# Kernel optimization log

Measured on AMD Instinct MI355X. Metric: run time of the kernel, lower is better.

## Reference

```python
import jax, jax.numpy as jnp
import numpy as np

N = 100000   # nodes
E = 600000   # edges
D_IN, D_H, D_OUT = 128, 128, 128


def glorot(key, shape):
    lim = float(np.sqrt(6.0 / (shape[0] + shape[1])))
    return jax.random.uniform(key, shape, jnp.float32, -lim, lim)


def setup_inputs() -> dict:
    key = jax.random.key(0)
    k1, k2, k3, k4 = jax.random.split(key, 4)
    x = jax.random.normal(k1, (N, D_IN), jnp.float32)
    edge_index = jax.random.randint(k2, (2, E), 0, N, jnp.int64)
    W1 = glorot(k3, (D_IN, D_H))
    b1 = jnp.zeros((D_H,), jnp.float32)
    W2 = glorot(k4, (D_H, D_OUT))
    b2 = jnp.zeros((D_OUT,), jnp.float32)
    return {"x": x, "W1": W1, "b1": b1, "W2": W2, "b2": b2, "edge_index": edge_index}


def gcn_conv(x, W, b, src, dst, n):
    # GCNConv: D^{-1/2}(A+I)D^{-1/2} X W + b  (self loops already in src/dst)
    h = x @ W                                   # [N, d_out]
    ones = jnp.ones(src.shape[0], h.dtype)
    deg = jax.ops.segment_sum(ones, dst, num_segments=n)      # in-degree incl self loop
    dinv = jnp.where(deg > 0, jax.lax.rsqrt(deg), 0.0)        # deg^{-1/2}
    norm = dinv[src] * dinv[dst]                              # [E+N]
    msgs = h[src] * norm[:, None]                             # gather + scale
    out = jax.ops.segment_sum(msgs, dst, num_segments=n)      # scatter-add to targets
    return out + b


def reference(x, W1, b1, W2, b2, edge_index):
    loop = jnp.arange(N, dtype=edge_index.dtype)
    src = jnp.concatenate([edge_index[0], loop])
    dst = jnp.concatenate([edge_index[1], loop])
    h = gcn_conv(x, W1, b1, src, dst, N)
    h = jax.nn.relu(h)  # dropout is a no-op in eval mode
    return gcn_conv(h, W2, b2, src, dst, N)
```

## Files before the change

kernel.cpp:

```cpp
#include <hip/hip_runtime.h>

#define NFEAT 128

typedef __attribute__((ext_vector_type(8))) short bf16x8;
typedef __attribute__((ext_vector_type(4))) float f32x4;

__device__ inline ushort f2b(float v) {
  unsigned u = __builtin_bit_cast(unsigned, v);
  return (ushort)((u + 0x7FFFu + ((u >> 16) & 1u)) >> 16);
}

__device__ inline void agg_accum(const ushort* __restrict__ h,
                                 const int2* __restrict__ csr2, int e, int end, int c,
                                 float& a0, float& a1, float& a2, float& a3) {
  for (; e < end; e += 4) {
    int4 q0 = *(const int4*)(csr2 + e);
    int4 q1 = *(const int4*)(csr2 + e + 2);
    uint2 h0 = *(const uint2*)(h + (size_t)q0.x * NFEAT + c);
    uint2 h1 = *(const uint2*)(h + (size_t)q0.z * NFEAT + c);
    uint2 h2 = *(const uint2*)(h + (size_t)q1.x * NFEAT + c);
    uint2 h3 = *(const uint2*)(h + (size_t)q1.z * NFEAT + c);
    float w0 = __int_as_float(q0.y), w1 = __int_as_float(q0.w);
    float w2 = __int_as_float(q1.y), w3 = __int_as_float(q1.w);
    a0 = fmaf(w0, __uint_as_float(h0.x << 16), a0);
    a1 = fmaf(w0, __uint_as_float(h0.x & 0xffff0000u), a1);
    a2 = fmaf(w0, __uint_as_float(h0.y << 16), a2);
    a3 = fmaf(w0, __uint_as_float(h0.y & 0xffff0000u), a3);
    a0 = fmaf(w1, __uint_as_float(h1.x << 16), a0);
    a1 = fmaf(w1, __uint_as_float(h1.x & 0xffff0000u), a1);
    a2 = fmaf(w1, __uint_as_float(h1.y << 16), a2);
    a3 = fmaf(w1, __uint_as_float(h1.y & 0xffff0000u), a3);
    a0 = fmaf(w2, __uint_as_float(h2.x << 16), a0);
    a1 = fmaf(w2, __uint_as_float(h2.x & 0xffff0000u), a1);
    a2 = fmaf(w2, __uint_as_float(h2.y << 16), a2);
    a3 = fmaf(w2, __uint_as_float(h2.y & 0xffff0000u), a3);
    a0 = fmaf(w3, __uint_as_float(h3.x << 16), a0);
    a1 = fmaf(w3, __uint_as_float(h3.x & 0xffff0000u), a1);
    a2 = fmaf(w3, __uint_as_float(h3.y << 16), a2);
    a3 = fmaf(w3, __uint_as_float(h3.y & 0xffff0000u), a3);
  }
}

__global__ __launch_bounds__(256) void k_cast_w(const float* __restrict__ W1,
                                                const float* __restrict__ W2,
                                                ushort* __restrict__ WT1,
                                                ushort* __restrict__ WT2) {
  int b = blockIdx.x;
  const float* W = (b < 64) ? W1 : W2;
  ushort* WT = (b < 64) ? WT1 : WT2;
  int idx = (b & 63) * 256 + threadIdx.x;
  int k = idx >> 7, nn = idx & 127;
  WT[nn * 128 + k] = f2b(W[idx]);
}


__global__ __launch_bounds__(256) void k_par1(const float* __restrict__ x,
                                              const ushort* __restrict__ WT1,
                                              ushort* __restrict__ h1, int n,
                                              const int* __restrict__ dst,
                                              int* __restrict__ cnt, int E,
                                              int gemmBlocks) {
  if ((int)blockIdx.x >= gemmBlocks) {
    int bid = blockIdx.x - gemmBlocks;
    int range = bid & 7, chunk = bid >> 3;
    int lo = (int)(((long long)range * n) >> 3);
    int hi = (int)(((long long)(range + 1) * n) >> 3);
    int i = chunk * 1024 + threadIdx.x * 4;
    if (i + 3 < E) {
      int4 d4 = *(const int4*)(dst + i);
      if ((unsigned)(d4.x - lo) < (unsigned)(hi - lo)) atomicAdd(&cnt[d4.x], 1);
      if ((unsigned)(d4.y - lo) < (unsigned)(hi - lo)) atomicAdd(&cnt[d4.y], 1);
      if ((unsigned)(d4.z - lo) < (unsigned)(hi - lo)) atomicAdd(&cnt[d4.z], 1);
      if ((unsigned)(d4.w - lo) < (unsigned)(hi - lo)) atomicAdd(&cnt[d4.w], 1);
    } else {
      for (int j = 0; j < 4; j++) {
        if (i + j < E) {
          int d = dst[i + j];
          if ((unsigned)(d - lo) < (unsigned)(hi - lo)) atomicAdd(&cnt[d], 1);
        }
      }
    }
    return;
  }
  __shared__ ushort sW[128][136];
  int tid = threadIdx.x;
  {
    int r = tid >> 1, hh = tid & 1;
    const uint4* srcp = (const uint4*)(WT1 + r * 128 + hh * 64);
    uint4* dstp = (uint4*)(&sW[r][hh * 64]);
#pragma unroll
    for (int j = 0; j < 8; j++) dstp[j] = srcp[j];
  }
  __syncthreads();

  int wave = tid >> 6;
  int lane = tid & 63;
  int l16 = lane & 15;
  int quad = lane >> 4;
  int rowBase = blockIdx.x * 128 + wave * 32;

  bf16x8 afrag[2][4];
#pragma unroll
  for (int rt = 0; rt < 2; rt++) {
    int row = rowBase + rt * 16 + l16;
    row = min(row, n - 1);
    const float* Ap = x + (size_t)row * NFEAT + quad * 8;
#pragma unroll
    for (int ks = 0; ks < 4; ks++) {
      float4 f0 = *(const float4*)(Ap + ks * 32);
      float4 f1 = *(const float4*)(Ap + ks * 32 + 4);
      ushort t[8] = {f2b(f0.x), f2b(f0.y), f2b(f0.z), f2b(f0.w),
                     f2b(f1.x), f2b(f1.y), f2b(f1.z), f2b(f1.w)};
      afrag[rt][ks] = *(const bf16x8*)t;
    }
  }

#pragma unroll
  for (int ct = 0; ct < 8; ct++) {
    bf16x8 bfrag[4];
#pragma unroll
    for (int ks = 0; ks < 4; ks++)
      bfrag[ks] = *(const bf16x8*)(&sW[ct * 16 + l16][ks * 32 + quad * 8]);
    f32x4 acc[2] = {{0.f, 0.f, 0.f, 0.f}, {0.f, 0.f, 0.f, 0.f}};
#pragma unroll
    for (int rt = 0; rt < 2; rt++)
#pragma unroll
      for (int ks = 0; ks < 4; ks++)
        acc[rt] = __builtin_amdgcn_mfma_f32_16x16x32_bf16(afrag[rt][ks], bfrag[ks],
                                                          acc[rt], 0, 0, 0);
#pragma unroll
    for (int rt = 0; rt < 2; rt++)
#pragma unroll
      for (int r = 0; r < 4; r++) {
        int row = rowBase + rt * 16 + quad * 4 + r;
        if (row < n) h1[(size_t)row * NFEAT + ct * 16 + l16] = f2b(acc[rt][r]);
      }
  }
}

__global__ __launch_bounds__(256) void k_scan_blocks(const int* __restrict__ cnt,
                                                     int* __restrict__ rowptr,
                                                     int* __restrict__ bsum,
                                                     float* __restrict__ dinv, int n) {
  __shared__ int s[256];
  int tid = threadIdx.x;
  int idx = blockIdx.x * 1024 + tid * 4;
  int v[4];
  int sum = 0;
#pragma unroll
  for (int j = 0; j < 4; j++) {
    int c = 0;
    if (idx + j < n) {
      c = cnt[idx + j];
      dinv[idx + j] = rsqrtf((float)(c + 1));
    }
    v[j] = (idx + j < n) ? ((c + 4) & ~3) : 0;
    sum += v[j];
  }
  s[tid] = sum;
  __syncthreads();
  for (int off = 1; off < 256; off <<= 1) {
    int t = (tid >= off) ? s[tid - off] : 0;
    __syncthreads();
    s[tid] += t;
    __syncthreads();
  }
  if (tid == 255) bsum[blockIdx.x] = s[255];
  int run = s[tid] - sum;
#pragma unroll
  for (int j = 0; j < 4; j++) {
    if (idx + j < n) rowptr[idx + j] = run;
    run += v[j];
  }
}

__global__ __launch_bounds__(256) void k_scan_addcur(int* __restrict__ rowptr,
                                                     const int* __restrict__ bsum,
                                                     int* __restrict__ cursor,
                                                     const float* __restrict__ dinv,
                                                     int2* __restrict__ csr2,
                                                     int n, int nb) {
  __shared__ int s[256];
  int tid = threadIdx.x;
  int v = (tid < nb) ? bsum[tid] : 0;
  s[tid] = v;
  __syncthreads();
  for (int off = 1; off < 256; off <<= 1) {
    int t = (tid >= off) ? s[tid - off] : 0;
    __syncthreads();
    s[tid] += t;
    __syncthreads();
  }
  int total = s[255];
  __syncthreads();
  int ex = s[tid] - v;
  __syncthreads();
  s[tid] = ex;
  __syncthreads();
  int range = blockIdx.x & 7, chunk = blockIdx.x >> 3;
  int lo = (int)(((long long)range * n) >> 3);
  int hi = (int)(((long long)(range + 1) * n) >> 3);
  int i = lo + chunk * 256 + tid;
  if (i < hi) {
    int rp = rowptr[i] + s[i >> 10];
    rowptr[i] = rp;
    cursor[i] = rp + 1;
    int2 self;
    self.x = i;
    self.y = __float_as_int(dinv[i]);
    csr2[rp] = self;
  }
  if (blockIdx.x == 0 && tid == 0) rowptr[n] = total;
}

__global__ __launch_bounds__(256) void k_scatter(const int* __restrict__ src,
                                                 const int* __restrict__ dst,
                                                 const float* __restrict__ dinv,
                                                 int* __restrict__ cursor,
                                                 int2* __restrict__ csr2, int E, int N) {
  int range = blockIdx.x & 7, chunk = blockIdx.x >> 3;
  int lo = (int)(((long long)range * N) >> 3);
  int hi = (int)(((long long)(range + 1) * N) >> 3);
  int i = chunk * 1024 + threadIdx.x * 4;
  if (i + 3 < E) {
    int4 d4 = *(const int4*)(dst + i);
    int4 s4 = *(const int4*)(src + i);
    int dd[4] = {d4.x, d4.y, d4.z, d4.w};
    int ss[4] = {s4.x, s4.y, s4.z, s4.w};
#pragma unroll
    for (int j = 0; j < 4; j++) {
      if ((unsigned)(dd[j] - lo) < (unsigned)(hi - lo)) {
        int p = atomicAdd(&cursor[dd[j]], 1);
        int2 v;
        v.x = ss[j];
        v.y = __float_as_int(dinv[ss[j]]);
        csr2[p] = v;
      }
    }
  } else {
    for (int j = 0; j < 4; j++) {
      if (i + j < E) {
        int d = dst[i + j];
        if ((unsigned)(d - lo) < (unsigned)(hi - lo)) {
          int s = src[i + j];
          int p = atomicAdd(&cursor[d], 1);
          int2 v;
          v.x = s;
          v.y = __float_as_int(dinv[s]);
          csr2[p] = v;
        }
      }
    }
  }
}


__global__ __launch_bounds__(256) void k_fused(const ushort* __restrict__ h1,
                                               const float* __restrict__ dinv,
                                               const int* __restrict__ rowptr,
                                               const int2* __restrict__ csr2,
                                               const float* __restrict__ b1,
                                               const ushort* __restrict__ WT2,
                                               ushort* __restrict__ h2, int n) {
  __shared__ ushort sW[128][136];
  __shared__ ushort sT[64][136];
  int tid = threadIdx.x;
  {
    int r = tid >> 1, hh = tid & 1;
    const uint4* srcp = (const uint4*)(WT2 + r * 128 + hh * 64);
    uint4* dstp = (uint4*)(&sW[r][hh * 64]);
#pragma unroll
    for (int j = 0; j < 8; j++) dstp[j] = srcp[j];
  }

  int base = blockIdx.x * 64;
  int c = (tid & 31) * 4;
#pragma unroll 1
  for (int batch = 0; batch < 8; batch++) {
    int nl = batch * 8 + (tid >> 5);
    int node = base + nl;
    if (node < n) {
      float a0 = 0.f, a1 = 0.f, a2 = 0.f, a3 = 0.f;
      agg_accum(h1, csr2, rowptr[node], rowptr[node + 1], c, a0, a1, a2, a3);
      float di = dinv[node];
      float4 bb = *(const float4*)(b1 + c);
      float o0 = fmaxf(fmaf(di, a0, bb.x), 0.f);
      float o1 = fmaxf(fmaf(di, a1, bb.y), 0.f);
      float o2 = fmaxf(fmaf(di, a2, bb.z), 0.f);
      float o3 = fmaxf(fmaf(di, a3, bb.w), 0.f);
      uint2 pk;
      pk.x = f2b(o0) | ((unsigned)f2b(o1) << 16);
      pk.y = f2b(o2) | ((unsigned)f2b(o3) << 16);
      *(uint2*)(&sT[nl][c]) = pk;
    }
  }
  __syncthreads();

  int wave = tid >> 6;
  int lane = tid & 63;
  int l16 = lane & 15;
  int quad = lane >> 4;
  bf16x8 afrag[4];
#pragma unroll
  for (int ks = 0; ks < 4; ks++)
    afrag[ks] = *(const bf16x8*)(&sT[wave * 16 + l16][ks * 32 + quad * 8]);

#pragma unroll
  for (int ct = 0; ct < 8; ct++) {
    bf16x8 bfrag[4];
#pragma unroll
    for (int ks = 0; ks < 4; ks++)
      bfrag[ks] = *(const bf16x8*)(&sW[ct * 16 + l16][ks * 32 + quad * 8]);
    f32x4 acc = {0.f, 0.f, 0.f, 0.f};
#pragma unroll
    for (int ks = 0; ks < 4; ks++)
      acc = __builtin_amdgcn_mfma_f32_16x16x32_bf16(afrag[ks], bfrag[ks], acc, 0, 0, 0);
#pragma unroll
    for (int r = 0; r < 4; r++) {
      int row = base + wave * 16 + quad * 4 + r;
      if (row < n) h2[(size_t)row * NFEAT + ct * 16 + l16] = f2b(acc[r]);
    }
  }
}


__global__ __launch_bounds__(256) void k_agg2(const ushort* __restrict__ h,
                                              const float* __restrict__ dinv,
                                              const int* __restrict__ rowptr,
                                              const int2* __restrict__ csr2,
                                              const float* __restrict__ bias,
                                              float* __restrict__ out, int n) {
  int node = blockIdx.x * 8 + (threadIdx.x >> 5);
  if (node >= n) return;
  int c = (threadIdx.x & 31) * 4;
  float a0 = 0.f, a1 = 0.f, a2 = 0.f, a3 = 0.f;
  agg_accum(h, csr2, rowptr[node], rowptr[node + 1], c, a0, a1, a2, a3);
  float di = dinv[node];
  float4 b = *(const float4*)(bias + c);
  float4 o;
  o.x = fmaf(di, a0, b.x);
  o.y = fmaf(di, a1, b.y);
  o.z = fmaf(di, a2, b.z);
  o.w = fmaf(di, a3, b.w);
  *(float4*)(out + (size_t)node * NFEAT + c) = o;
}


extern "C" void kernel_launch(void* const* d_in, const int* in_sizes, int n_in,
                              void* d_out, int out_size, void* d_ws, size_t ws_size,
                              hipStream_t stream) {
  const float* x = (const float*)d_in[0];
  const float* W1 = (const float*)d_in[1];
  const float* b1 = (const float*)d_in[2];
  const float* W2 = (const float*)d_in[3];
  const float* b2 = (const float*)d_in[4];
  const int* ei = (const int*)d_in[5];

  const int N = in_sizes[0] / NFEAT;
  const int E = in_sizes[5] / 2;
  const int* srcIdx = ei;
  const int* dstIdx = ei + E;

  char* p = (char*)d_ws;
  auto alloc = [&](size_t bytes) {
    char* r = p;
    p += (bytes + 255) & ~(size_t)255;
    return r;
  };
  int* cnt = (int*)alloc((size_t)N * 4);
  int2* csr2 = (int2*)alloc((size_t)(E + 4 * N + 16) * 8);
  char* memset_end = p;
  int* cursor = (int*)alloc((size_t)N * 4);
  float* dinv = (float*)alloc((size_t)N * 4);
  int* rowptr = (int*)alloc((size_t)(N + 1) * 4);
  int* bsum = (int*)alloc(1024);
  ushort* WT1 = (ushort*)alloc(NFEAT * NFEAT * 2);
  ushort* WT2 = (ushort*)alloc(NFEAT * NFEAT * 2);
  ushort* h2 = (ushort*)alloc((size_t)N * NFEAT * 2);
  ushort* h1 = (ushort*)d_out;
  float* out = (float*)d_out;

  hipMemsetAsync(cnt, 0, (size_t)(memset_end - (char*)cnt), stream);

  int nb = (N + 1023) / 1024;
  int gEx = ((E + 1023) / 1024) * 8;
  int gG1 = (N + 127) / 128;
  int cpr = (((N + 7) / 8) + 255) / 256;

  k_cast_w<<<128, 256, 0, stream>>>(W1, W2, WT1, WT2);
  k_par1<<<gG1 + gEx, 256, 0, stream>>>(x, WT1, h1, N, dstIdx, cnt, E, gG1);
  k_scan_blocks<<<nb, 256, 0, stream>>>(cnt, rowptr, bsum, dinv, N);
  k_scan_addcur<<<8 * cpr, 256, 0, stream>>>(rowptr, bsum, cursor, dinv, csr2, N, nb);
  k_scatter<<<gEx, 256, 0, stream>>>(srcIdx, dstIdx, dinv, cursor, csr2, E, N);
  k_fused<<<(N + 63) / 64, 256, 0, stream>>>(h1, dinv, rowptr, csr2, b1, WT2, h2, N);
  k_agg2<<<(N + 7) / 8, 256, 0, stream>>>(h2, dinv, rowptr, csr2, b2, out, N);
}
```

Baseline: 276.4 us.

## Split fused layer-1 aggregation and layer-2 GEMM into separate kernels

Replaces the fused kernel, which aggregated 64 nodes into shared memory and then ran the second GEMM, with two kernels. A plain aggregation kernel (8 nodes per block) writes the ReLU'd bf16 intermediate to a new global buffer, and a standalone MFMA GEMM kernel then reads it. This removes the fused kernel's large shared-memory footprint, its per-block weight load and its serial 8-batch loop, so occupancy and load balance should improve for the gather-bound aggregation. The cost is an extra 25.6 MB write and read of the intermediate plus one more launch.

```diff
diff --git a/kernel.cpp b/kernel.cpp
--- a/kernel.cpp
+++ b/kernel.cpp
@@ -138,6 +138,60 @@
   }
 }
 
+
+__global__ __launch_bounds__(256) void k_gemm2(const ushort* __restrict__ A,
+                                               const ushort* __restrict__ WT,
+                                               ushort* __restrict__ out, int n) {
+  __shared__ ushort sW[128][136];
+  int tid = threadIdx.x;
+  {
+    int r = tid >> 1, hh = tid & 1;
+    const uint4* srcp = (const uint4*)(WT + r * 128 + hh * 64);
+    uint4* dstp = (uint4*)(&sW[r][hh * 64]);
+#pragma unroll
+    for (int j = 0; j < 8; j++) dstp[j] = srcp[j];
+  }
+  __syncthreads();
+
+  int wave = tid >> 6;
+  int lane = tid & 63;
+  int l16 = lane & 15;
+  int quad = lane >> 4;
+  int rowBase = blockIdx.x * 128 + wave * 32;
+
+  bf16x8 afrag[2][4];
+#pragma unroll
+  for (int rt = 0; rt < 2; rt++) {
+    int row = rowBase + rt * 16 + l16;
+    row = min(row, n - 1);
+    const ushort* Ap = A + (size_t)row * NFEAT + quad * 8;
+#pragma unroll
+    for (int ks = 0; ks < 4; ks++) afrag[rt][ks] = *(const bf16x8*)(Ap + ks * 32);
+  }
+
+#pragma unroll
+  for (int ct = 0; ct < 8; ct++) {
+    bf16x8 bfrag[4];
+#pragma unroll
+    for (int ks = 0; ks < 4; ks++)
+      bfrag[ks] = *(const bf16x8*)(&sW[ct * 16 + l16][ks * 32 + quad * 8]);
+    f32x4 acc[2] = {{0.f, 0.f, 0.f, 0.f}, {0.f, 0.f, 0.f, 0.f}};
+#pragma unroll
+    for (int rt = 0; rt < 2; rt++)
+#pragma unroll
+      for (int ks = 0; ks < 4; ks++)
+        acc[rt] = __builtin_amdgcn_mfma_f32_16x16x32_bf16(afrag[rt][ks], bfrag[ks],
+                                                          acc[rt], 0, 0, 0);
+#pragma unroll
+    for (int rt = 0; rt < 2; rt++)
+#pragma unroll
+      for (int r = 0; r < 4; r++) {
+        int row = rowBase + rt * 16 + quad * 4 + r;
+        if (row < n) out[(size_t)row * NFEAT + ct * 16 + l16] = f2b(acc[rt][r]);
+      }
+  }
+}
+
 __global__ __launch_bounds__(256) void k_scan_blocks(const int* __restrict__ cnt,
                                                      int* __restrict__ rowptr,
                                                      int* __restrict__ bsum,
@@ -255,72 +309,27 @@
 }
 
 
-__global__ __launch_bounds__(256) void k_fused(const ushort* __restrict__ h1,
-                                               const float* __restrict__ dinv,
-                                               const int* __restrict__ rowptr,
-                                               const int2* __restrict__ csr2,
-                                               const float* __restrict__ b1,
-                                               const ushort* __restrict__ WT2,
-                                               ushort* __restrict__ h2, int n) {
-  __shared__ ushort sW[128][136];
-  __shared__ ushort sT[64][136];
-  int tid = threadIdx.x;
-  {
-    int r = tid >> 1, hh = tid & 1;
-    const uint4* srcp = (const uint4*)(WT2 + r * 128 + hh * 64);
-    uint4* dstp = (uint4*)(&sW[r][hh * 64]);
-#pragma unroll
-    for (int j = 0; j < 8; j++) dstp[j] = srcp[j];
-  }
-
-  int base = blockIdx.x * 64;
-  int c = (tid & 31) * 4;
-#pragma unroll 1
-  for (int batch = 0; batch < 8; batch++) {
-    int nl = batch * 8 + (tid >> 5);
-    int node = base + nl;
-    if (node < n) {
-      float a0 = 0.f, a1 = 0.f, a2 = 0.f, a3 = 0.f;
-      agg_accum(h1, csr2, rowptr[node], rowptr[node + 1], c, a0, a1, a2, a3);
-      float di = dinv[node];
-      float4 bb = *(const float4*)(b1 + c);
-      float o0 = fmaxf(fmaf(di, a0, bb.x), 0.f);
-      float o1 = fmaxf(fmaf(di, a1, bb.y), 0.f);
-      float o2 = fmaxf(fmaf(di, a2, bb.z), 0.f);
-      float o3 = fmaxf(fmaf(di, a3, bb.w), 0.f);
-      uint2 pk;
-      pk.x = f2b(o0) | ((unsigned)f2b(o1) << 16);
-      pk.y = f2b(o2) | ((unsigned)f2b(o3) << 16);
-      *(uint2*)(&sT[nl][c]) = pk;
-    }
-  }
-  __syncthreads();
-
-  int wave = tid >> 6;
-  int lane = tid & 63;
-  int l16 = lane & 15;
-  int quad = lane >> 4;
-  bf16x8 afrag[4];
-#pragma unroll
-  for (int ks = 0; ks < 4; ks++)
-    afrag[ks] = *(const bf16x8*)(&sT[wave * 16 + l16][ks * 32 + quad * 8]);
-
-#pragma unroll
-  for (int ct = 0; ct < 8; ct++) {
-    bf16x8 bfrag[4];
-#pragma unroll
-    for (int ks = 0; ks < 4; ks++)
-      bfrag[ks] = *(const bf16x8*)(&sW[ct * 16 + l16][ks * 32 + quad * 8]);
-    f32x4 acc = {0.f, 0.f, 0.f, 0.f};
-#pragma unroll
-    for (int ks = 0; ks < 4; ks++)
-      acc = __builtin_amdgcn_mfma_f32_16x16x32_bf16(afrag[ks], bfrag[ks], acc, 0, 0, 0);
-#pragma unroll
-    for (int r = 0; r < 4; r++) {
-      int row = base + wave * 16 + quad * 4 + r;
-      if (row < n) h2[(size_t)row * NFEAT + ct * 16 + l16] = f2b(acc[r]);
-    }
-  }
+__global__ __launch_bounds__(256) void k_agg1(const ushort* __restrict__ h,
+                                              const float* __restrict__ dinv,
+                                              const int* __restrict__ rowptr,
+                                              const int2* __restrict__ csr2,
+                                              const float* __restrict__ bias,
+                                              ushort* __restrict__ out, int n) {
+  int node = blockIdx.x * 8 + (threadIdx.x >> 5);
+  if (node >= n) return;
+  int c = (threadIdx.x & 31) * 4;
+  float a0 = 0.f, a1 = 0.f, a2 = 0.f, a3 = 0.f;
+  agg_accum(h, csr2, rowptr[node], rowptr[node + 1], c, a0, a1, a2, a3);
+  float di = dinv[node];
+  float4 b = *(const float4*)(bias + c);
+  float o0 = fmaxf(fmaf(di, a0, b.x), 0.f);
+  float o1 = fmaxf(fmaf(di, a1, b.y), 0.f);
+  float o2 = fmaxf(fmaf(di, a2, b.z), 0.f);
+  float o3 = fmaxf(fmaf(di, a3, b.w), 0.f);
+  uint2 pk;
+  pk.x = f2b(o0) | ((unsigned)f2b(o1) << 16);
+  pk.y = f2b(o2) | ((unsigned)f2b(o3) << 16);
+  *(uint2*)(out + (size_t)node * NFEAT + c) = pk;
 }
 
 
@@ -376,6 +385,7 @@
   int* bsum = (int*)alloc(1024);
   ushort* WT1 = (ushort*)alloc(NFEAT * NFEAT * 2);
   ushort* WT2 = (ushort*)alloc(NFEAT * NFEAT * 2);
+  ushort* t1 = (ushort*)alloc((size_t)N * NFEAT * 2);
   ushort* h2 = (ushort*)alloc((size_t)N * NFEAT * 2);
   ushort* h1 = (ushort*)d_out;
   float* out = (float*)d_out;
@@ -384,14 +394,15 @@
 
   int nb = (N + 1023) / 1024;
   int gEx = ((E + 1023) / 1024) * 8;
-  int gG1 = (N + 127) / 128;
+  int gG = (N + 127) / 128;
   int cpr = (((N + 7) / 8) + 255) / 256;
 
   k_cast_w<<<128, 256, 0, stream>>>(W1, W2, WT1, WT2);
-  k_par1<<<gG1 + gEx, 256, 0, stream>>>(x, WT1, h1, N, dstIdx, cnt, E, gG1);
+  k_par1<<<gG + gEx, 256, 0, stream>>>(x, WT1, h1, N, dstIdx, cnt, E, gG);
   k_scan_blocks<<<nb, 256, 0, stream>>>(cnt, rowptr, bsum, dinv, N);
   k_scan_addcur<<<8 * cpr, 256, 0, stream>>>(rowptr, bsum, cursor, dinv, csr2, N, nb);
   k_scatter<<<gEx, 256, 0, stream>>>(srcIdx, dstIdx, dinv, cursor, csr2, E, N);
-  k_fused<<<(N + 63) / 64, 256, 0, stream>>>(h1, dinv, rowptr, csr2, b1, WT2, h2, N);
+  k_agg1<<<(N + 7) / 8, 256, 0, stream>>>(h1, dinv, rowptr, csr2, b1, t1, N);
+  k_gemm2<<<gG, 256, 0, stream>>>(t1, WT2, h2, N);
   k_agg2<<<(N + 7) / 8, 256, 0, stream>>>(h2, dinv, rowptr, csr2, b2, out, N);
 }
```

New measurement: 251.6 us. 9.0% less time.
